# Performance work log

Measured on AMD Instinct MI355X. Metric: run time of the kernel, lower is better.

Reference implementation:

```python
import jax, jax.numpy as jnp
import numpy as np

B, A, D, H = 2048, 32, 128, 256

def setup_inputs() -> dict:
    key = jax.random.key(0)
    ks = jax.random.split(key, 12)
    s = lambda fan_in: 1.0 / np.sqrt(fan_in)
    return {
        "obs": jax.random.normal(ks[0], (B, A, D), dtype=jnp.float32),
        "act": jax.random.normal(ks[1], (B, A, 8), dtype=jnp.float32),
        "enc_W": jax.random.uniform(ks[2], (H, D), jnp.float32, -s(D), s(D)),
        "enc_b": jax.random.uniform(ks[3], (H,), jnp.float32, -s(D), s(D)),
        "fobs_W": jax.random.uniform(ks[4], (H, H), jnp.float32, -s(H), s(H)),
        "fobs_b": jax.random.uniform(ks[5], (H,), jnp.float32, -s(H), s(H)),
        "W_ih": jax.random.uniform(ks[6], (3 * H, H), jnp.float32, -s(H), s(H)),
        "b_ih": jax.random.uniform(ks[7], (3 * H,), jnp.float32, -s(H), s(H)),
        "W_hh": jax.random.uniform(ks[8], (3 * H, H), jnp.float32, -s(H), s(H)),
        "b_hh": jax.random.uniform(ks[9], (3 * H,), jnp.float32, -s(H), s(H)),
        "dec_W": jax.random.uniform(ks[10], (1, H), jnp.float32, -s(H), s(H)),
        "dec_b": jax.random.uniform(ks[11], (1,), jnp.float32, -s(H), s(H)),
    }

def _gru_cell(x, h, W_ih, b_ih, W_hh, b_hh):
    # torch.nn.GRUCell: gates stacked as [reset, update, new]
    gi = x @ W_ih.T + b_ih          # [N, 3H]
    gh = h @ W_hh.T + b_hh          # [N, 3H]
    i_r, i_z, i_n = jnp.split(gi, 3, axis=-1)
    h_r, h_z, h_n = jnp.split(gh, 3, axis=-1)
    r = jax.nn.sigmoid(i_r + h_r)
    z = jax.nn.sigmoid(i_z + h_z)
    n = jnp.tanh(i_n + r * h_n)
    return (1.0 - z) * n + z * h

def reference(obs, act, enc_W, enc_b, fobs_W, fobs_b, W_ih, b_ih, W_hh, b_hh, dec_W, dec_b):
    b, a, d = obs.shape
    x = obs.reshape(b * a, d)                         # [B*A, D]
    e = jax.nn.relu(x @ enc_W.T + enc_b)              # encoder + ReLU
    h = e @ fobs_W.T + fobs_b                         # h_out
    # k = 0: comm input is zeros
    h = _gru_cell(jnp.zeros_like(h), h, W_ih, b_ih, W_hh, b_hh)
    # k = 1: masked mean over other agents == (sum_j h_j - h_i) / n_agents
    hA = h.reshape(b, a, -1)                          # [B, A, H]
    c = (hA.sum(axis=1, keepdims=True) - hA) / a      # [B, A, H]
    h = _gru_cell(c.reshape(b * a, -1), h, W_ih, b_ih, W_hh, b_hh)
    return (h @ dec_W.T + dec_b).reshape(b, a, -1)    # [B, A, 1]
```

## Files before the change

### kernel.cpp

```cpp
#include <hip/hip_runtime.h>
#include <hip/hip_fp16.h>


#define NB   2048
#define NA   32
#define DIN  128
#define HID  256
#define SA   264

typedef _Float16 half8  __attribute__((ext_vector_type(8)));
typedef float    float4v __attribute__((ext_vector_type(4)));

#define ENC_OFF    0
#define FOBS_OFF   32768
#define WIH_OFF    98304
#define WHH_OFF    294912
#define PREP_TOTAL 491520

__global__ void prep_weights(const float* __restrict__ encW, const float* __restrict__ fobsW,
                             const float* __restrict__ wih,  const float* __restrict__ whh,
                             _Float16* __restrict__ prep) {
    int F = blockIdx.x * 256 + threadIdx.x;
    if (F >= PREP_TOTAL) return;
    const float* src; int K, NT, local = F;
    if (F < FOBS_OFF)     { src = encW;  K = 128; NT = 16; }
    else if (F < WIH_OFF) { src = fobsW; K = 256; NT = 16; local = F - FOBS_OFF; }
    else if (F < WHH_OFF) { src = wih;   K = 256; NT = 48; local = F - WIH_OFF; }
    else                  { src = whh;   K = 256; NT = 48; local = F - WHH_OFF; }
    int j    = local & 7;
    int lane = (local >> 3) & 63;
    int t    = local >> 9;
    int nt   = t % NT;
    int ks   = t / NT;
    int col  = nt * 16 + (lane & 15);
    int k    = ks * 32 + ((lane >> 4) << 3) + j;
    prep[F] = (_Float16)src[col * K + k];
}

__device__ __forceinline__ float sigmoid_f(float x) {
    x = fminf(fmaxf(x, -30.f), 30.f);
    return 1.f / (1.f + __expf(-x));
}
__device__ __forceinline__ float tanh_f(float x) {
    x = fminf(fmaxf(x, -15.f), 15.f);
    float e = __expf(-2.f * x);
    return (1.f - e) / (1.f + e);
}

__device__ __forceinline__ void zero22(float4v a[2][2]) {
    float4v z = {0.f, 0.f, 0.f, 0.f};
    a[0][0] = z; a[0][1] = z; a[1][0] = z; a[1][1] = z;
}

__device__ __forceinline__ half8 ldB(const _Float16* __restrict__ prepm, int NT, int nt, int ks,
                                     const float* __restrict__ raw, int K, int use_prep, int lane) {
    if (use_prep)
        return *(const half8*)(prepm + (((ks * NT + nt) * 64 + lane) << 3));
    half8 b;
    int l16 = lane & 15, kq = (lane >> 4) << 3;
    #pragma unroll
    for (int j = 0; j < 8; j++)
        b[j] = (_Float16)raw[(nt * 16 + l16) * K + ks * 32 + kq + j];
    return b;
}

template<int KSTEPS>
__device__ __forceinline__ void gemm_tile(const _Float16* __restrict__ Abuf,
        const _Float16* __restrict__ prepm, int NT, int ntg0,
        const float* __restrict__ raw, int K, int use_prep,
        int lane, float4v acc[2][2])
{
    const int l16 = lane & 15;
    const int kq  = (lane >> 4) << 3;
    #pragma unroll
    for (int ks = 0; ks < KSTEPS; ks++) {
        int kbase = ks * 32 + kq;
        half8 a0 = *(const half8*)(Abuf + l16 * SA + kbase);
        half8 a1 = *(const half8*)(Abuf + (16 + l16) * SA + kbase);
        half8 b0 = ldB(prepm, NT, ntg0,     ks, raw, K, use_prep, lane);
        half8 b1 = ldB(prepm, NT, ntg0 + 1, ks, raw, K, use_prep, lane);
        acc[0][0] = __builtin_amdgcn_mfma_f32_16x16x32_f16(a0, b0, acc[0][0], 0, 0, 0);
        acc[0][1] = __builtin_amdgcn_mfma_f32_16x16x32_f16(a0, b1, acc[0][1], 0, 0, 0);
        acc[1][0] = __builtin_amdgcn_mfma_f32_16x16x32_f16(a1, b0, acc[1][0], 0, 0, 0);
        acc[1][1] = __builtin_amdgcn_mfma_f32_16x16x32_f16(a1, b1, acc[1][1], 0, 0, 0);
    }
}

__global__ __launch_bounds__(512) void commnet_fused(
    const float* __restrict__ obs, const _Float16* __restrict__ prep,
    const float* __restrict__ enc_b, const float* __restrict__ fobs_b,
    const float* __restrict__ b_ih, const float* __restrict__ b_hh,
    const float* __restrict__ dec_W, const float* __restrict__ dec_b,
    float* __restrict__ out,
    const float* __restrict__ encW, const float* __restrict__ fobsW,
    const float* __restrict__ wih, const float* __restrict__ whh,
    int use_prep)
{
    const int b    = blockIdx.x;
    const int tid  = threadIdx.x;
    const int lane = tid & 63;
    const int w    = tid >> 6;
    const int l16  = lane & 15;
    const int quad = lane >> 4;
    const int kq   = quad << 3;
    const int ntl0 = w * 2;

    __shared__ __align__(16) _Float16 sA[2][NA * SA];
    __shared__ __align__(16) float S[HID];

    {
        const float* obsb = obs + (size_t)b * NA * DIN;
        int r   = tid >> 4;
        int off = (tid & 15) << 3;
        const float* src = obsb + r * DIN + off;
        float4v v0 = *(const float4v*)(src);
        float4v v1 = *(const float4v*)(src + 4);
        half8 hv;
        hv[0] = (_Float16)v0[0]; hv[1] = (_Float16)v0[1];
        hv[2] = (_Float16)v0[2]; hv[3] = (_Float16)v0[3];
        hv[4] = (_Float16)v1[0]; hv[5] = (_Float16)v1[1];
        hv[6] = (_Float16)v1[2]; hv[7] = (_Float16)v1[3];
        *(half8*)(&sA[0][r * SA + off]) = hv;
    }
    __syncthreads();

    float4v acc[2][2];

    zero22(acc);
    gemm_tile<4>(&sA[0][0], prep + ENC_OFF, 16, ntl0, encW, DIN, use_prep, lane, acc);
    #pragma unroll
    for (int nn = 0; nn < 2; nn++) {
        int col = (ntl0 + nn) * 16 + l16;
        float bb = enc_b[col];
        #pragma unroll
        for (int mt = 0; mt < 2; mt++)
            #pragma unroll
            for (int r = 0; r < 4; r++) {
                int row = mt * 16 + quad * 4 + r;
                float v = acc[mt][nn][r] + bb;
                sA[1][row * SA + col] = (_Float16)fmaxf(v, 0.f);
            }
    }
    __syncthreads();

    zero22(acc);
    gemm_tile<8>(&sA[1][0], prep + FOBS_OFF, 16, ntl0, fobsW, HID, use_prep, lane, acc);
    #pragma unroll
    for (int nn = 0; nn < 2; nn++) {
        int col = (ntl0 + nn) * 16 + l16;
        float bb = fobs_b[col];
        #pragma unroll
        for (int mt = 0; mt < 2; mt++)
            #pragma unroll
            for (int r = 0; r < 4; r++) {
                int row = mt * 16 + quad * 4 + r;
                sA[0][row * SA + col] = (_Float16)(acc[mt][nn][r] + bb);
            }
    }
    __syncthreads();

    {
        float4v aR[2][2], aZ[2][2], aN[2][2];
        zero22(aR); zero22(aZ); zero22(aN);
        #pragma unroll 2
        for (int ks = 0; ks < 8; ks++) {
            const int kbase = ks * 32 + kq;
            half8 a0 = *(const half8*)(&sA[0][l16 * SA + kbase]);
            half8 a1 = *(const half8*)(&sA[0][(16 + l16) * SA + kbase]);
            half8 bR0 = ldB(prep + WHH_OFF, 48,  0 + ntl0,     ks, whh, HID, use_prep, lane);
            half8 bR1 = ldB(prep + WHH_OFF, 48,  0 + ntl0 + 1, ks, whh, HID, use_prep, lane);
            half8 bZ0 = ldB(prep + WHH_OFF, 48, 16 + ntl0,     ks, whh, HID, use_prep, lane);
            half8 bZ1 = ldB(prep + WHH_OFF, 48, 16 + ntl0 + 1, ks, whh, HID, use_prep, lane);
            half8 bN0 = ldB(prep + WHH_OFF, 48, 32 + ntl0,     ks, whh, HID, use_prep, lane);
            half8 bN1 = ldB(prep + WHH_OFF, 48, 32 + ntl0 + 1, ks, whh, HID, use_prep, lane);
            aR[0][0] = __builtin_amdgcn_mfma_f32_16x16x32_f16(a0, bR0, aR[0][0], 0, 0, 0);
            aR[0][1] = __builtin_amdgcn_mfma_f32_16x16x32_f16(a0, bR1, aR[0][1], 0, 0, 0);
            aR[1][0] = __builtin_amdgcn_mfma_f32_16x16x32_f16(a1, bR0, aR[1][0], 0, 0, 0);
            aR[1][1] = __builtin_amdgcn_mfma_f32_16x16x32_f16(a1, bR1, aR[1][1], 0, 0, 0);
            aZ[0][0] = __builtin_amdgcn_mfma_f32_16x16x32_f16(a0, bZ0, aZ[0][0], 0, 0, 0);
            aZ[0][1] = __builtin_amdgcn_mfma_f32_16x16x32_f16(a0, bZ1, aZ[0][1], 0, 0, 0);
            aZ[1][0] = __builtin_amdgcn_mfma_f32_16x16x32_f16(a1, bZ0, aZ[1][0], 0, 0, 0);
            aZ[1][1] = __builtin_amdgcn_mfma_f32_16x16x32_f16(a1, bZ1, aZ[1][1], 0, 0, 0);
            aN[0][0] = __builtin_amdgcn_mfma_f32_16x16x32_f16(a0, bN0, aN[0][0], 0, 0, 0);
            aN[0][1] = __builtin_amdgcn_mfma_f32_16x16x32_f16(a0, bN1, aN[0][1], 0, 0, 0);
            aN[1][0] = __builtin_amdgcn_mfma_f32_16x16x32_f16(a1, bN0, aN[1][0], 0, 0, 0);
            aN[1][1] = __builtin_amdgcn_mfma_f32_16x16x32_f16(a1, bN1, aN[1][1], 0, 0, 0);
        }
        #pragma unroll
        for (int nn = 0; nn < 2; nn++) {
            int col = (ntl0 + nn) * 16 + l16;
            float biR = b_ih[col],       bhR = b_hh[col];
            float biZ = b_ih[256 + col], bhZ = b_hh[256 + col];
            float biN = b_ih[512 + col], bhN = b_hh[512 + col];
            float ssum = 0.f;
            #pragma unroll
            for (int mt = 0; mt < 2; mt++)
                #pragma unroll
                for (int r = 0; r < 4; r++) {
                    int row = mt * 16 + quad * 4 + r;
                    float rg = sigmoid_f(biR + aR[mt][nn][r] + bhR);
                    float zg = sigmoid_f(biZ + aZ[mt][nn][r] + bhZ);
                    float ng = tanh_f(biN + rg * (aN[mt][nn][r] + bhN));
                    float hold = (float)sA[0][row * SA + col];
                    float h1 = (1.f - zg) * ng + zg * hold;
                    sA[1][row * SA + col] = (_Float16)h1;
                    ssum += h1;
                }
            ssum += __shfl_xor(ssum, 16);
            ssum += __shfl_xor(ssum, 32);
            if (lane < 16) S[col] = ssum;
        }
    }
    __syncthreads();

    for (int i = tid; i < (NA * HID) / 8; i += 512) {
        int r  = i >> 5;
        int c8 = (i & 31) << 3;
        half8 hv = *(const half8*)(&sA[1][r * SA + c8]);
        float4v s0 = *(const float4v*)(&S[c8]);
        float4v s1 = *(const float4v*)(&S[c8 + 4]);
        half8 cv;
        cv[0] = (_Float16)((s0[0] - (float)hv[0]) * (1.f / 32.f));
        cv[1] = (_Float16)((s0[1] - (float)hv[1]) * (1.f / 32.f));
        cv[2] = (_Float16)((s0[2] - (float)hv[2]) * (1.f / 32.f));
        cv[3] = (_Float16)((s0[3] - (float)hv[3]) * (1.f / 32.f));
        cv[4] = (_Float16)((s1[0] - (float)hv[4]) * (1.f / 32.f));
        cv[5] = (_Float16)((s1[1] - (float)hv[5]) * (1.f / 32.f));
        cv[6] = (_Float16)((s1[2] - (float)hv[6]) * (1.f / 32.f));
        cv[7] = (_Float16)((s1[3] - (float)hv[7]) * (1.f / 32.f));
        *(half8*)(&sA[0][r * SA + c8]) = cv;
    }
    __syncthreads();
    if (tid < NA) S[tid] = 0.f;
    __syncthreads();

    {
        float4v aR[2][2], aZ[2][2], aNi[2][2], aNh[2][2];
        zero22(aR); zero22(aZ); zero22(aNi); zero22(aNh);
        #pragma unroll 2
        for (int ks = 0; ks < 8; ks++) {
            const int kbase = ks * 32 + kq;
            half8 c0 = *(const half8*)(&sA[0][l16 * SA + kbase]);
            half8 c1 = *(const half8*)(&sA[0][(16 + l16) * SA + kbase]);
            half8 bIR0 = ldB(prep + WIH_OFF, 48,  0 + ntl0,     ks, wih, HID, use_prep, lane);
            half8 bIR1 = ldB(prep + WIH_OFF, 48,  0 + ntl0 + 1, ks, wih, HID, use_prep, lane);
            half8 bIZ0 = ldB(prep + WIH_OFF, 48, 16 + ntl0,     ks, wih, HID, use_prep, lane);
            half8 bIZ1 = ldB(prep + WIH_OFF, 48, 16 + ntl0 + 1, ks, wih, HID, use_prep, lane);
            half8 bIN0 = ldB(prep + WIH_OFF, 48, 32 + ntl0,     ks, wih, HID, use_prep, lane);
            half8 bIN1 = ldB(prep + WIH_OFF, 48, 32 + ntl0 + 1, ks, wih, HID, use_prep, lane);
            aR[0][0]  = __builtin_amdgcn_mfma_f32_16x16x32_f16(c0, bIR0, aR[0][0], 0, 0, 0);
            aR[0][1]  = __builtin_amdgcn_mfma_f32_16x16x32_f16(c0, bIR1, aR[0][1], 0, 0, 0);
            aR[1][0]  = __builtin_amdgcn_mfma_f32_16x16x32_f16(c1, bIR0, aR[1][0], 0, 0, 0);
            aR[1][1]  = __builtin_amdgcn_mfma_f32_16x16x32_f16(c1, bIR1, aR[1][1], 0, 0, 0);
            aZ[0][0]  = __builtin_amdgcn_mfma_f32_16x16x32_f16(c0, bIZ0, aZ[0][0], 0, 0, 0);
            aZ[0][1]  = __builtin_amdgcn_mfma_f32_16x16x32_f16(c0, bIZ1, aZ[0][1], 0, 0, 0);
            aZ[1][0]  = __builtin_amdgcn_mfma_f32_16x16x32_f16(c1, bIZ0, aZ[1][0], 0, 0, 0);
            aZ[1][1]  = __builtin_amdgcn_mfma_f32_16x16x32_f16(c1, bIZ1, aZ[1][1], 0, 0, 0);
            aNi[0][0] = __builtin_amdgcn_mfma_f32_16x16x32_f16(c0, bIN0, aNi[0][0], 0, 0, 0);
            aNi[0][1] = __builtin_amdgcn_mfma_f32_16x16x32_f16(c0, bIN1, aNi[0][1], 0, 0, 0);
            aNi[1][0] = __builtin_amdgcn_mfma_f32_16x16x32_f16(c1, bIN0, aNi[1][0], 0, 0, 0);
            aNi[1][1] = __builtin_amdgcn_mfma_f32_16x16x32_f16(c1, bIN1, aNi[1][1], 0, 0, 0);
            half8 h0 = *(const half8*)(&sA[1][l16 * SA + kbase]);
            half8 h1f = *(const half8*)(&sA[1][(16 + l16) * SA + kbase]);
            half8 bHR0 = ldB(prep + WHH_OFF, 48,  0 + ntl0,     ks, whh, HID, use_prep, lane);
            half8 bHR1 = ldB(prep + WHH_OFF, 48,  0 + ntl0 + 1, ks, whh, HID, use_prep, lane);
            half8 bHZ0 = ldB(prep + WHH_OFF, 48, 16 + ntl0,     ks, whh, HID, use_prep, lane);
            half8 bHZ1 = ldB(prep + WHH_OFF, 48, 16 + ntl0 + 1, ks, whh, HID, use_prep, lane);
            half8 bHN0 = ldB(prep + WHH_OFF, 48, 32 + ntl0,     ks, whh, HID, use_prep, lane);
            half8 bHN1 = ldB(prep + WHH_OFF, 48, 32 + ntl0 + 1, ks, whh, HID, use_prep, lane);
            aR[0][0]  = __builtin_amdgcn_mfma_f32_16x16x32_f16(h0,  bHR0, aR[0][0], 0, 0, 0);
            aR[0][1]  = __builtin_amdgcn_mfma_f32_16x16x32_f16(h0,  bHR1, aR[0][1], 0, 0, 0);
            aR[1][0]  = __builtin_amdgcn_mfma_f32_16x16x32_f16(h1f, bHR0, aR[1][0], 0, 0, 0);
            aR[1][1]  = __builtin_amdgcn_mfma_f32_16x16x32_f16(h1f, bHR1, aR[1][1], 0, 0, 0);
            aZ[0][0]  = __builtin_amdgcn_mfma_f32_16x16x32_f16(h0,  bHZ0, aZ[0][0], 0, 0, 0);
            aZ[0][1]  = __builtin_amdgcn_mfma_f32_16x16x32_f16(h0,  bHZ1, aZ[0][1], 0, 0, 0);
            aZ[1][0]  = __builtin_amdgcn_mfma_f32_16x16x32_f16(h1f, bHZ0, aZ[1][0], 0, 0, 0);
            aZ[1][1]  = __builtin_amdgcn_mfma_f32_16x16x32_f16(h1f, bHZ1, aZ[1][1], 0, 0, 0);
            aNh[0][0] = __builtin_amdgcn_mfma_f32_16x16x32_f16(h0,  bHN0, aNh[0][0], 0, 0, 0);
            aNh[0][1] = __builtin_amdgcn_mfma_f32_16x16x32_f16(h0,  bHN1, aNh[0][1], 0, 0, 0);
            aNh[1][0] = __builtin_amdgcn_mfma_f32_16x16x32_f16(h1f, bHN0, aNh[1][0], 0, 0, 0);
            aNh[1][1] = __builtin_amdgcn_mfma_f32_16x16x32_f16(h1f, bHN1, aNh[1][1], 0, 0, 0);
        }

        float dw0 = dec_W[(ntl0    ) * 16 + l16];
        float dw1 = dec_W[(ntl0 + 1) * 16 + l16];
        float p[2][4];
        #pragma unroll
        for (int mt = 0; mt < 2; mt++)
            #pragma unroll
            for (int r = 0; r < 4; r++)
                p[mt][r] = 0.f;
        #pragma unroll
        for (int nn = 0; nn < 2; nn++) {
            int col = (ntl0 + nn) * 16 + l16;
            float biR = b_ih[col],       bhR = b_hh[col];
            float biZ = b_ih[256 + col], bhZ = b_hh[256 + col];
            float biN = b_ih[512 + col], bhN = b_hh[512 + col];
            float dw = nn ? dw1 : dw0;
            #pragma unroll
            for (int mt = 0; mt < 2; mt++)
                #pragma unroll
                for (int r = 0; r < 4; r++) {
                    int row = mt * 16 + quad * 4 + r;
                    float rg = sigmoid_f(aR[mt][nn][r] + biR + bhR);
                    float zg = sigmoid_f(aZ[mt][nn][r] + biZ + bhZ);
                    float ng = tanh_f((aNi[mt][nn][r] + biN) + rg * (aNh[mt][nn][r] + bhN));
                    float h1v = (float)sA[1][row * SA + col];
                    float h2 = (1.f - zg) * ng + zg * h1v;
                    p[mt][r] += h2 * dw;
                }
        }
        #pragma unroll
        for (int m = 1; m <= 8; m <<= 1) {
            #pragma unroll
            for (int mt = 0; mt < 2; mt++)
                #pragma unroll
                for (int r = 0; r < 4; r++)
                    p[mt][r] += __shfl_xor(p[mt][r], m);
        }
        if (l16 == 0) {
            #pragma unroll
            for (int mt = 0; mt < 2; mt++)
                #pragma unroll
                for (int r = 0; r < 4; r++)
                    atomicAdd(&S[mt * 16 + quad * 4 + r], p[mt][r]);
        }
    }
    __syncthreads();
    if (tid < NA) out[(size_t)b * NA + tid] = S[tid] + dec_b[0];
}

extern "C" void kernel_launch(void* const* d_in, const int* in_sizes, int n_in,
                              void* d_out, int out_size, void* d_ws, size_t ws_size,
                              hipStream_t stream) {
    const float* obs   = (const float*)d_in[0];
    const float* encW  = (const float*)d_in[2];
    const float* encb  = (const float*)d_in[3];
    const float* fobsW = (const float*)d_in[4];
    const float* fobsb = (const float*)d_in[5];
    const float* wih   = (const float*)d_in[6];
    const float* bih   = (const float*)d_in[7];
    const float* whh   = (const float*)d_in[8];
    const float* bhh   = (const float*)d_in[9];
    const float* decW  = (const float*)d_in[10];
    const float* decb  = (const float*)d_in[11];
    float* out = (float*)d_out;

    _Float16* prep = (_Float16*)d_ws;
    int use_prep = (ws_size >= (size_t)PREP_TOTAL * sizeof(_Float16)) ? 1 : 0;
    if (use_prep) {
        prep_weights<<<(PREP_TOTAL + 255) / 256, 256, 0, stream>>>(encW, fobsW, wih, whh, prep);
    }
    commnet_fused<<<NB, 512, 0, stream>>>(obs, prep, encb, fobsb, bih, bhh, decW, decb, out,
                                          encW, fobsW, wih, whh, use_prep);
}
```

Before: 275.5 us.

## Process two batch elements per block with 16 waves, each owning one column tile

Each workgroup now handles two batch elements (64 rows) with 1024 threads, and each of the 16 waves computes one 16-column tile across four 16-row M tiles instead of two column tiles over two M tiles. The intent is to halve the number of weight (B-operand) loads per MFMA, so each weight fragment fetched from global/L2 is reused across four row tiles, and to halve the block count. Per-agent-group sums are kept separately for the two batch elements. Shared memory doubles and 1024-thread blocks may reduce occupancy and scheduling flexibility.

```diff
diff --git a/kernel.cpp b/kernel.cpp
--- a/kernel.cpp
+++ b/kernel.cpp
@@ -7,6 +7,7 @@
 #define DIN  128
 #define HID  256
 #define SA   264
+#define MROWS 64
 
 typedef _Float16 half8  __attribute__((ext_vector_type(8)));
 typedef float    float4v __attribute__((ext_vector_type(4)));
@@ -47,11 +48,6 @@
     return (1.f - e) / (1.f + e);
 }
 
-__device__ __forceinline__ void zero22(float4v a[2][2]) {
-    float4v z = {0.f, 0.f, 0.f, 0.f};
-    a[0][0] = z; a[0][1] = z; a[1][0] = z; a[1][1] = z;
-}
-
 __device__ __forceinline__ half8 ldB(const _Float16* __restrict__ prepm, int NT, int nt, int ks,
                                      const float* __restrict__ raw, int K, int use_prep, int lane) {
     if (use_prep)
@@ -65,28 +61,28 @@
 }
 
 template<int KSTEPS>
-__device__ __forceinline__ void gemm_tile(const _Float16* __restrict__ Abuf,
-        const _Float16* __restrict__ prepm, int NT, int ntg0,
+__device__ __forceinline__ void gemm_col16(const _Float16* __restrict__ Abuf,
+        const _Float16* __restrict__ prepm, int NT, int nt,
         const float* __restrict__ raw, int K, int use_prep,
-        int lane, float4v acc[2][2])
+        int lane, float4v acc[4])
 {
     const int l16 = lane & 15;
     const int kq  = (lane >> 4) << 3;
-    #pragma unroll
+    #pragma unroll 2
     for (int ks = 0; ks < KSTEPS; ks++) {
         int kbase = ks * 32 + kq;
-        half8 a0 = *(const half8*)(Abuf + l16 * SA + kbase);
-        half8 a1 = *(const half8*)(Abuf + (16 + l16) * SA + kbase);
-        half8 b0 = ldB(prepm, NT, ntg0,     ks, raw, K, use_prep, lane);
-        half8 b1 = ldB(prepm, NT, ntg0 + 1, ks, raw, K, use_prep, lane);
-        acc[0][0] = __builtin_amdgcn_mfma_f32_16x16x32_f16(a0, b0, acc[0][0], 0, 0, 0);
-        acc[0][1] = __builtin_amdgcn_mfma_f32_16x16x32_f16(a0, b1, acc[0][1], 0, 0, 0);
-        acc[1][0] = __builtin_amdgcn_mfma_f32_16x16x32_f16(a1, b0, acc[1][0], 0, 0, 0);
-        acc[1][1] = __builtin_amdgcn_mfma_f32_16x16x32_f16(a1, b1, acc[1][1], 0, 0, 0);
-    }
-}
-
-__global__ __launch_bounds__(512) void commnet_fused(
+        half8 Af[4];
+        #pragma unroll
+        for (int mt = 0; mt < 4; mt++)
+            Af[mt] = *(const half8*)(Abuf + (mt * 16 + l16) * SA + kbase);
+        half8 b0 = ldB(prepm, NT, nt, ks, raw, K, use_prep, lane);
+        #pragma unroll
+        for (int mt = 0; mt < 4; mt++)
+            acc[mt] = __builtin_amdgcn_mfma_f32_16x16x32_f16(Af[mt], b0, acc[mt], 0, 0, 0);
+    }
+}
+
+__global__ __launch_bounds__(1024) void commnet_fused(
     const float* __restrict__ obs, const _Float16* __restrict__ prep,
     const float* __restrict__ enc_b, const float* __restrict__ fobs_b,
     const float* __restrict__ b_ih, const float* __restrict__ b_hh,
@@ -103,13 +99,14 @@
     const int l16  = lane & 15;
     const int quad = lane >> 4;
     const int kq   = quad << 3;
-    const int ntl0 = w * 2;
-
-    __shared__ __align__(16) _Float16 sA[2][NA * SA];
-    __shared__ __align__(16) float S[HID];
-
-    {
-        const float* obsb = obs + (size_t)b * NA * DIN;
+    const int col  = w * 16 + l16;
+
+    __shared__ __align__(16) _Float16 sA[2][MROWS * SA];
+    __shared__ __align__(16) float S[2][HID];
+    __shared__ float Srow[MROWS];
+
+    {
+        const float* obsb = obs + (size_t)b * MROWS * DIN;
         int r   = tid >> 4;
         int off = (tid & 15) << 3;
         const float* src = obsb + r * DIN + off;
@@ -124,210 +121,195 @@
     }
     __syncthreads();
 
-    float4v acc[2][2];
-
-    zero22(acc);
-    gemm_tile<4>(&sA[0][0], prep + ENC_OFF, 16, ntl0, encW, DIN, use_prep, lane, acc);
-    #pragma unroll
-    for (int nn = 0; nn < 2; nn++) {
-        int col = (ntl0 + nn) * 16 + l16;
+    float4v acc[4];
+
+    {
+        float4v z = {0.f, 0.f, 0.f, 0.f};
+        acc[0] = z; acc[1] = z; acc[2] = z; acc[3] = z;
+        gemm_col16<4>(&sA[0][0], prep + ENC_OFF, 16, w, encW, DIN, use_prep, lane, acc);
         float bb = enc_b[col];
         #pragma unroll
-        for (int mt = 0; mt < 2; mt++)
+        for (int mt = 0; mt < 4; mt++)
             #pragma unroll
             for (int r = 0; r < 4; r++) {
                 int row = mt * 16 + quad * 4 + r;
-                float v = acc[mt][nn][r] + bb;
-                sA[1][row * SA + col] = (_Float16)fmaxf(v, 0.f);
-            }
-    }
-    __syncthreads();
-
-    zero22(acc);
-    gemm_tile<8>(&sA[1][0], prep + FOBS_OFF, 16, ntl0, fobsW, HID, use_prep, lane, acc);
-    #pragma unroll
-    for (int nn = 0; nn < 2; nn++) {
-        int col = (ntl0 + nn) * 16 + l16;
+                sA[1][row * SA + col] = (_Float16)fmaxf(acc[mt][r] + bb, 0.f);
+            }
+    }
+    __syncthreads();
+
+    {
+        float4v z = {0.f, 0.f, 0.f, 0.f};
+        acc[0] = z; acc[1] = z; acc[2] = z; acc[3] = z;
+        gemm_col16<8>(&sA[1][0], prep + FOBS_OFF, 16, w, fobsW, HID, use_prep, lane, acc);
         float bb = fobs_b[col];
         #pragma unroll
-        for (int mt = 0; mt < 2; mt++)
+        for (int mt = 0; mt < 4; mt++)
             #pragma unroll
             for (int r = 0; r < 4; r++) {
                 int row = mt * 16 + quad * 4 + r;
-                sA[0][row * SA + col] = (_Float16)(acc[mt][nn][r] + bb);
-            }
-    }
-    __syncthreads();
-
-    {
-        float4v aR[2][2], aZ[2][2], aN[2][2];
-        zero22(aR); zero22(aZ); zero22(aN);
+                sA[0][row * SA + col] = (_Float16)(acc[mt][r] + bb);
+            }
+    }
+    __syncthreads();
+
+    {
+        float4v aR[4], aZ[4], aN[4];
+        float4v z = {0.f, 0.f, 0.f, 0.f};
+        #pragma unroll
+        for (int mt = 0; mt < 4; mt++) { aR[mt] = z; aZ[mt] = z; aN[mt] = z; }
         #pragma unroll 2
         for (int ks = 0; ks < 8; ks++) {
             const int kbase = ks * 32 + kq;
-            half8 a0 = *(const half8*)(&sA[0][l16 * SA + kbase]);
-            half8 a1 = *(const half8*)(&sA[0][(16 + l16) * SA + kbase]);
-            half8 bR0 = ldB(prep + WHH_OFF, 48,  0 + ntl0,     ks, whh, HID, use_prep, lane);
-            half8 bR1 = ldB(prep + WHH_OFF, 48,  0 + ntl0 + 1, ks, whh, HID, use_prep, lane);
-            half8 bZ0 = ldB(prep + WHH_OFF, 48, 16 + ntl0,     ks, whh, HID, use_prep, lane);
-            half8 bZ1 = ldB(prep + WHH_OFF, 48, 16 + ntl0 + 1, ks, whh, HID, use_prep, lane);
-            half8 bN0 = ldB(prep + WHH_OFF, 48, 32 + ntl0,     ks, whh, HID, use_prep, lane);
-            half8 bN1 = ldB(prep + WHH_OFF, 48, 32 + ntl0 + 1, ks, whh, HID, use_prep, lane);
-            aR[0][0] = __builtin_amdgcn_mfma_f32_16x16x32_f16(a0, bR0, aR[0][0], 0, 0, 0);
-            aR[0][1] = __builtin_amdgcn_mfma_f32_16x16x32_f16(a0, bR1, aR[0][1], 0, 0, 0);
-            aR[1][0] = __builtin_amdgcn_mfma_f32_16x16x32_f16(a1, bR0, aR[1][0], 0, 0, 0);
-            aR[1][1] = __builtin_amdgcn_mfma_f32_16x16x32_f16(a1, bR1, aR[1][1], 0, 0, 0);
-            aZ[0][0] = __builtin_amdgcn_mfma_f32_16x16x32_f16(a0, bZ0, aZ[0][0], 0, 0, 0);
-            aZ[0][1] = __builtin_amdgcn_mfma_f32_16x16x32_f16(a0, bZ1, aZ[0][1], 0, 0, 0);
-            aZ[1][0] = __builtin_amdgcn_mfma_f32_16x16x32_f16(a1, bZ0, aZ[1][0], 0, 0, 0);
-            aZ[1][1] = __builtin_amdgcn_mfma_f32_16x16x32_f16(a1, bZ1, aZ[1][1], 0, 0, 0);
-            aN[0][0] = __builtin_amdgcn_mfma_f32_16x16x32_f16(a0, bN0, aN[0][0], 0, 0, 0);
-            aN[0][1] = __builtin_amdgcn_mfma_f32_16x16x32_f16(a0, bN1, aN[0][1], 0, 0, 0);
-            aN[1][0] = __builtin_amdgcn_mfma_f32_16x16x32_f16(a1, bN0, aN[1][0], 0, 0, 0);
-            aN[1][1] = __builtin_amdgcn_mfma_f32_16x16x32_f16(a1, bN1, aN[1][1], 0, 0, 0);
-        }
-        #pragma unroll
-        for (int nn = 0; nn < 2; nn++) {
-            int col = (ntl0 + nn) * 16 + l16;
-            float biR = b_ih[col],       bhR = b_hh[col];
-            float biZ = b_ih[256 + col], bhZ = b_hh[256 + col];
-            float biN = b_ih[512 + col], bhN = b_hh[512 + col];
-            float ssum = 0.f;
-            #pragma unroll
-            for (int mt = 0; mt < 2; mt++)
-                #pragma unroll
-                for (int r = 0; r < 4; r++) {
-                    int row = mt * 16 + quad * 4 + r;
-                    float rg = sigmoid_f(biR + aR[mt][nn][r] + bhR);
-                    float zg = sigmoid_f(biZ + aZ[mt][nn][r] + bhZ);
-                    float ng = tanh_f(biN + rg * (aN[mt][nn][r] + bhN));
-                    float hold = (float)sA[0][row * SA + col];
-                    float h1 = (1.f - zg) * ng + zg * hold;
-                    sA[1][row * SA + col] = (_Float16)h1;
-                    ssum += h1;
-                }
-            ssum += __shfl_xor(ssum, 16);
-            ssum += __shfl_xor(ssum, 32);
-            if (lane < 16) S[col] = ssum;
-        }
-    }
-    __syncthreads();
-
-    for (int i = tid; i < (NA * HID) / 8; i += 512) {
-        int r  = i >> 5;
-        int c8 = (i & 31) << 3;
-        half8 hv = *(const half8*)(&sA[1][r * SA + c8]);
-        float4v s0 = *(const float4v*)(&S[c8]);
-        float4v s1 = *(const float4v*)(&S[c8 + 4]);
-        half8 cv;
-        cv[0] = (_Float16)((s0[0] - (float)hv[0]) * (1.f / 32.f));
-        cv[1] = (_Float16)((s0[1] - (float)hv[1]) * (1.f / 32.f));
-        cv[2] = (_Float16)((s0[2] - (float)hv[2]) * (1.f / 32.f));
-        cv[3] = (_Float16)((s0[3] - (float)hv[3]) * (1.f / 32.f));
-        cv[4] = (_Float16)((s1[0] - (float)hv[4]) * (1.f / 32.f));
-        cv[5] = (_Float16)((s1[1] - (float)hv[5]) * (1.f / 32.f));
-        cv[6] = (_Float16)((s1[2] - (float)hv[6]) * (1.f / 32.f));
-        cv[7] = (_Float16)((s1[3] - (float)hv[7]) * (1.f / 32.f));
-        *(half8*)(&sA[0][r * SA + c8]) = cv;
-    }
-    __syncthreads();
-    if (tid < NA) S[tid] = 0.f;
-    __syncthreads();
-
-    {
-        float4v aR[2][2], aZ[2][2], aNi[2][2], aNh[2][2];
-        zero22(aR); zero22(aZ); zero22(aNi); zero22(aNh);
+            half8 Af[4];
+            #pragma unroll
+            for (int mt = 0; mt < 4; mt++)
+                Af[mt] = *(const half8*)(&sA[0][(mt * 16 + l16) * SA + kbase]);
+            half8 bR = ldB(prep + WHH_OFF, 48,  0 + w, ks, whh, HID, use_prep, lane);
+            half8 bZ = ldB(prep + WHH_OFF, 48, 16 + w, ks, whh, HID, use_prep, lane);
+            half8 bN = ldB(prep + WHH_OFF, 48, 32 + w, ks, whh, HID, use_prep, lane);
+            #pragma unroll
+            for (int mt = 0; mt < 4; mt++)
+                aR[mt] = __builtin_amdgcn_mfma_f32_16x16x32_f16(Af[mt], bR, aR[mt], 0, 0, 0);
+            #pragma unroll
+            for (int mt = 0; mt < 4; mt++)
+                aZ[mt] = __builtin_amdgcn_mfma_f32_16x16x32_f16(Af[mt], bZ, aZ[mt], 0, 0, 0);
+            #pragma unroll
+            for (int mt = 0; mt < 4; mt++)
+                aN[mt] = __builtin_amdgcn_mfma_f32_16x16x32_f16(Af[mt], bN, aN[mt], 0, 0, 0);
+        }
+        float biR = b_ih[col],       bhR = b_hh[col];
+        float biZ = b_ih[256 + col], bhZ = b_hh[256 + col];
+        float biN = b_ih[512 + col], bhN = b_hh[512 + col];
+        float s0 = 0.f, s1 = 0.f;
+        #pragma unroll
+        for (int mt = 0; mt < 4; mt++) {
+            float psum = 0.f;
+            #pragma unroll
+            for (int r = 0; r < 4; r++) {
+                int row = mt * 16 + quad * 4 + r;
+                float rg = sigmoid_f(biR + aR[mt][r] + bhR);
+                float zg = sigmoid_f(biZ + aZ[mt][r] + bhZ);
+                float ng = tanh_f(biN + rg * (aN[mt][r] + bhN));
+                float hold = (float)sA[0][row * SA + col];
+                float h1 = (1.f - zg) * ng + zg * hold;
+                sA[1][row * SA + col] = (_Float16)h1;
+                psum += h1;
+            }
+            if (mt < 2) s0 += psum; else s1 += psum;
+        }
+        s0 += __shfl_xor(s0, 16); s0 += __shfl_xor(s0, 32);
+        s1 += __shfl_xor(s1, 16); s1 += __shfl_xor(s1, 32);
+        if (lane < 16) { S[0][col] = s0; S[1][col] = s1; }
+    }
+    __syncthreads();
+
+    {
+        #pragma unroll
+        for (int it = 0; it < 2; it++) {
+            int i  = tid + it * 1024;
+            int r  = i >> 5;
+            int c8 = (i & 31) << 3;
+            const float* Sp = &S[r >> 5][0];
+            half8 hv = *(const half8*)(&sA[1][r * SA + c8]);
+            float4v t0 = *(const float4v*)(Sp + c8);
+            float4v t1 = *(const float4v*)(Sp + c8 + 4);
+            half8 cv;
+            cv[0] = (_Float16)((t0[0] - (float)hv[0]) * (1.f / 32.f));
+            cv[1] = (_Float16)((t0[1] - (float)hv[1]) * (1.f / 32.f));
+            cv[2] = (_Float16)((t0[2] - (float)hv[2]) * (1.f / 32.f));
+            cv[3] = (_Float16)((t0[3] - (float)hv[3]) * (1.f / 32.f));
+            cv[4] = (_Float16)((t1[0] - (float)hv[4]) * (1.f / 32.f));
+            cv[5] = (_Float16)((t1[1] - (float)hv[5]) * (1.f / 32.f));
+            cv[6] = (_Float16)((t1[2] - (float)hv[6]) * (1.f / 32.f));
+            cv[7] = (_Float16)((t1[3] - (float)hv[7]) * (1.f / 32.f));
+            *(half8*)(&sA[0][r * SA + c8]) = cv;
+        }
+        if (tid < MROWS) Srow[tid] = 0.f;
+    }
+    __syncthreads();
+
+    {
+        float4v aR[4], aZ[4], aNi[4], aNh[4];
+        float4v z = {0.f, 0.f, 0.f, 0.f};
+        #pragma unroll
+        for (int mt = 0; mt < 4; mt++) { aR[mt] = z; aZ[mt] = z; aNi[mt] = z; aNh[mt] = z; }
         #pragma unroll 2
         for (int ks = 0; ks < 8; ks++) {
             const int kbase = ks * 32 + kq;
-            half8 c0 = *(const half8*)(&sA[0][l16 * SA + kbase]);
-            half8 c1 = *(const half8*)(&sA[0][(16 + l16) * SA + kbase]);
-            half8 bIR0 = ldB(prep + WIH_OFF, 48,  0 + ntl0,     ks, wih, HID, use_prep, lane);
-            half8 bIR1 = ldB(prep + WIH_OFF, 48,  0 + ntl0 + 1, ks, wih, HID, use_prep, lane);
-            half8 bIZ0 = ldB(prep + WIH_OFF, 48, 16 + ntl0,     ks, wih, HID, use_prep, lane);
-            half8 bIZ1 = ldB(prep + WIH_OFF, 48, 16 + ntl0 + 1, ks, wih, HID, use_prep, lane);
-            half8 bIN0 = ldB(prep + WIH_OFF, 48, 32 + ntl0,     ks, wih, HID, use_prep, lane);
-            half8 bIN1 = ldB(prep + WIH_OFF, 48, 32 + ntl0 + 1, ks, wih, HID, use_prep, lane);
-            aR[0][0]  = __builtin_amdgcn_mfma_f32_16x16x32_f16(c0, bIR0, aR[0][0], 0, 0, 0);
-            aR[0][1]  = __builtin_amdgcn_mfma_f32_16x16x32_f16(c0, bIR1, aR[0][1], 0, 0, 0);
-            aR[1][0]  = __builtin_amdgcn_mfma_f32_16x16x32_f16(c1, bIR0, aR[1][0], 0, 0, 0);
-            aR[1][1]  = __builtin_amdgcn_mfma_f32_16x16x32_f16(c1, bIR1, aR[1][1], 0, 0, 0);
-            aZ[0][0]  = __builtin_amdgcn_mfma_f32_16x16x32_f16(c0, bIZ0, aZ[0][0], 0, 0, 0);
-            aZ[0][1]  = __builtin_amdgcn_mfma_f32_16x16x32_f16(c0, bIZ1, aZ[0][1], 0, 0, 0);
-            aZ[1][0]  = __builtin_amdgcn_mfma_f32_16x16x32_f16(c1, bIZ0, aZ[1][0], 0, 0, 0);
-            aZ[1][1]  = __builtin_amdgcn_mfma_f32_16x16x32_f16(c1, bIZ1, aZ[1][1], 0, 0, 0);
-            aNi[0][0] = __builtin_amdgcn_mfma_f32_16x16x32_f16(c0, bIN0, aNi[0][0], 0, 0, 0);
-            aNi[0][1] = __builtin_amdgcn_mfma_f32_16x16x32_f16(c0, bIN1, aNi[0][1], 0, 0, 0);
-            aNi[1][0] = __builtin_amdgcn_mfma_f32_16x16x32_f16(c1, bIN0, aNi[1][0], 0, 0, 0);
-            aNi[1][1] = __builtin_amdgcn_mfma_f32_16x16x32_f16(c1, bIN1, aNi[1][1], 0, 0, 0);
-            half8 h0 = *(const half8*)(&sA[1][l16 * SA + kbase]);
-            half8 h1f = *(const half8*)(&sA[1][(16 + l16) * SA + kbase]);
-            half8 bHR0 = ldB(prep + WHH_OFF, 48,  0 + ntl0,     ks, whh, HID, use_prep, lane);
-            half8 bHR1 = ldB(prep + WHH_OFF, 48,  0 + ntl0 + 1, ks, whh, HID, use_prep, lane);
-            half8 bHZ0 = ldB(prep + WHH_OFF, 48, 16 + ntl0,     ks, whh, HID, use_prep, lane);
-            half8 bHZ1 = ldB(prep + WHH_OFF, 48, 16 + ntl0 + 1, ks, whh, HID, use_prep, lane);
-            half8 bHN0 = ldB(prep + WHH_OFF, 48, 32 + ntl0,     ks, whh, HID, use_prep, lane);
-            half8 bHN1 = ldB(prep + WHH_OFF, 48, 32 + ntl0 + 1, ks, whh, HID, use_prep, lane);
-            aR[0][0]  = __builtin_amdgcn_mfma_f32_16x16x32_f16(h0,  bHR0, aR[0][0], 0, 0, 0);
-            aR[0][1]  = __builtin_amdgcn_mfma_f32_16x16x32_f16(h0,  bHR1, aR[0][1], 0, 0, 0);
-            aR[1][0]  = __builtin_amdgcn_mfma_f32_16x16x32_f16(h1f, bHR0, aR[1][0], 0, 0, 0);
-            aR[1][1]  = __builtin_amdgcn_mfma_f32_16x16x32_f16(h1f, bHR1, aR[1][1], 0, 0, 0);
-            aZ[0][0]  = __builtin_amdgcn_mfma_f32_16x16x32_f16(h0,  bHZ0, aZ[0][0], 0, 0, 0);
-            aZ[0][1]  = __builtin_amdgcn_mfma_f32_16x16x32_f16(h0,  bHZ1, aZ[0][1], 0, 0, 0);
-            aZ[1][0]  = __builtin_amdgcn_mfma_f32_16x16x32_f16(h1f, bHZ0, aZ[1][0], 0, 0, 0);
-            aZ[1][1]  = __builtin_amdgcn_mfma_f32_16x16x32_f16(h1f, bHZ1, aZ[1][1], 0, 0, 0);
-            aNh[0][0] = __builtin_amdgcn_mfma_f32_16x16x32_f16(h0,  bHN0, aNh[0][0], 0, 0, 0);
-            aNh[0][1] = __builtin_amdgcn_mfma_f32_16x16x32_f16(h0,  bHN1, aNh[0][1], 0, 0, 0);
-            aNh[1][0] = __builtin_amdgcn_mfma_f32_16x16x32_f16(h1f, bHN0, aNh[1][0], 0, 0, 0);
-            aNh[1][1] = __builtin_amdgcn_mfma_f32_16x16x32_f16(h1f, bHN1, aNh[1][1], 0, 0, 0);
-        }
-
-        float dw0 = dec_W[(ntl0    ) * 16 + l16];
-        float dw1 = dec_W[(ntl0 + 1) * 16 + l16];
-        float p[2][4];
-        #pragma unroll
-        for (int mt = 0; mt < 2; mt++)
-            #pragma unroll
-            for (int r = 0; r < 4; r++)
-                p[mt][r] = 0.f;
-        #pragma unroll
-        for (int nn = 0; nn < 2; nn++) {
-            int col = (ntl0 + nn) * 16 + l16;
-            float biR = b_ih[col],       bhR = b_hh[col];
-            float biZ = b_ih[256 + col], bhZ = b_hh[256 + col];
-            float biN = b_ih[512 + col], bhN = b_hh[512 + col];
-            float dw = nn ? dw1 : dw0;
-            #pragma unroll
-            for (int mt = 0; mt < 2; mt++)
-                #pragma unroll
-                for (int r = 0; r < 4; r++) {
-                    int row = mt * 16 + quad * 4 + r;
-                    float rg = sigmoid_f(aR[mt][nn][r] + biR + bhR);
-                    float zg = sigmoid_f(aZ[mt][nn][r] + biZ + bhZ);
-                    float ng = tanh_f((aNi[mt][nn][r] + biN) + rg * (aNh[mt][nn][r] + bhN));
-                    float h1v = (float)sA[1][row * SA + col];
-                    float h2 = (1.f - zg) * ng + zg * h1v;
-                    p[mt][r] += h2 * dw;
-                }
-        }
+            {
+                half8 Cf[4];
+                #pragma unroll
+                for (int mt = 0; mt < 4; mt++)
+                    Cf[mt] = *(const half8*)(&sA[0][(mt * 16 + l16) * SA + kbase]);
+                half8 bR = ldB(prep + WIH_OFF, 48,  0 + w, ks, wih, HID, use_prep, lane);
+                half8 bZ = ldB(prep + WIH_OFF, 48, 16 + w, ks, wih, HID, use_prep, lane);
+                half8 bN = ldB(prep + WIH_OFF, 48, 32 + w, ks, wih, HID, use_prep, lane);
+                #pragma unroll
+                for (int mt = 0; mt < 4; mt++)
+                    aR[mt]  = __builtin_amdgcn_mfma_f32_16x16x32_f16(Cf[mt], bR, aR[mt], 0, 0, 0);
+                #pragma unroll
+                for (int mt = 0; mt < 4; mt++)
+                    aZ[mt]  = __builtin_amdgcn_mfma_f32_16x16x32_f16(Cf[mt], bZ, aZ[mt], 0, 0, 0);
+                #pragma unroll
+                for (int mt = 0; mt < 4; mt++)
+                    aNi[mt] = __builtin_amdgcn_mfma_f32_16x16x32_f16(Cf[mt], bN, aNi[mt], 0, 0, 0);
+            }
+            {
+                half8 Hf[4];
+                #pragma unroll
+                for (int mt = 0; mt < 4; mt++)
+                    Hf[mt] = *(const half8*)(&sA[1][(mt * 16 + l16) * SA + kbase]);
+                half8 bR = ldB(prep + WHH_OFF, 48,  0 + w, ks, whh, HID, use_prep, lane);
+                half8 bZ = ldB(prep + WHH_OFF, 48, 16 + w, ks, whh, HID, use_prep, lane);
+                half8 bN = ldB(prep + WHH_OFF, 48, 32 + w, ks, whh, HID, use_prep, lane);
+                #pragma unroll
+                for (int mt = 0; mt < 4; mt++)
+                    aR[mt]  = __builtin_amdgcn_mfma_f32_16x16x32_f16(Hf[mt], bR, aR[mt], 0, 0, 0);
+                #pragma unroll
+                for (int mt = 0; mt < 4; mt++)
+                    aZ[mt]  = __builtin_amdgcn_mfma_f32_16x16x32_f16(Hf[mt], bZ, aZ[mt], 0, 0, 0);
+                #pragma unroll
+                for (int mt = 0; mt < 4; mt++)
+                    aNh[mt] = __builtin_amdgcn_mfma_f32_16x16x32_f16(Hf[mt], bN, aNh[mt], 0, 0, 0);
+            }
+        }
+
+        float biR = b_ih[col],       bhR = b_hh[col];
+        float biZ = b_ih[256 + col], bhZ = b_hh[256 + col];
+        float biN = b_ih[512 + col], bhN = b_hh[512 + col];
+        float dw  = dec_W[col];
+        float p[4][4];
+        #pragma unroll
+        for (int mt = 0; mt < 4; mt++)
+            #pragma unroll
+            for (int r = 0; r < 4; r++) {
+                int row = mt * 16 + quad * 4 + r;
+                float rg = sigmoid_f(aR[mt][r] + biR + bhR);
+                float zg = sigmoid_f(aZ[mt][r] + biZ + bhZ);
+                float ng = tanh_f((aNi[mt][r] + biN) + rg * (aNh[mt][r] + bhN));
+                float h1v = (float)sA[1][row * SA + col];
+                float h2 = (1.f - zg) * ng + zg * h1v;
+                p[mt][r] = h2 * dw;
+            }
         #pragma unroll
         for (int m = 1; m <= 8; m <<= 1) {
             #pragma unroll
-            for (int mt = 0; mt < 2; mt++)
+            for (int mt = 0; mt < 4; mt++)
                 #pragma unroll
                 for (int r = 0; r < 4; r++)
                     p[mt][r] += __shfl_xor(p[mt][r], m);
         }
         if (l16 == 0) {
             #pragma unroll
-            for (int mt = 0; mt < 2; mt++)
+            for (int mt = 0; mt < 4; mt++)
                 #pragma unroll
                 for (int r = 0; r < 4; r++)
-                    atomicAdd(&S[mt * 16 + quad * 4 + r], p[mt][r]);
-        }
-    }
-    __syncthreads();
-    if (tid < NA) out[(size_t)b * NA + tid] = S[tid] + dec_b[0];
+                    atomicAdd(&Srow[mt * 16 + quad * 4 + r], p[mt][r]);
+        }
+    }
+    __syncthreads();
+    if (tid < MROWS) out[(size_t)b * MROWS + tid] = Srow[tid] + dec_b[0];
 }
 
 extern "C" void kernel_launch(void* const* d_in, const int* in_sizes, int n_in,
@@ -351,6 +333,6 @@
     if (use_prep) {
         prep_weights<<<(PREP_TOTAL + 255) / 256, 256, 0, stream>>>(encW, fobsW, wih, whh, prep);
     }
-    commnet_fused<<<NB, 512, 0, stream>>>(obs, prep, encb, fobsb, bih, bhh, decW, decb, out,
-                                          encW, fobsW, wih, whh, use_prep);
-}
+    commnet_fused<<<NB / 2, 1024, 0, stream>>>(obs, prep, encb, fobsb, bih, bhh, decW, decb, out,
+                                               encW, fobsW, wih, whh, use_prep);
+}
```

Result: faster. 247.8 us (-10.0%).
